# Performance work log

Measured on AMD Instinct MI355X. Metric: run time of the kernel, lower is better.

The kernel has to match this reference:

```python
import jax, jax.numpy as jnp
import numpy as np

B, N, D, H, E, W, OUT = 4, 2048, 128, 4, 32768, 8, 128


def setup_inputs() -> dict:
    key = jax.random.key(0)
    ks = jax.random.split(key, 11)
    s = 0.05  # weight init scale
    return {
        "nodefeatures": jax.random.normal(ks[0], (B, N, D), jnp.float32),
        "node_indices": jax.random.randint(ks[1], (B, 2, E), 0, N),
        "nodeattributes": jax.random.uniform(ks[2], (B, E, W), jnp.float32),
        "wq_w": jax.random.normal(ks[3], (H, D, D), jnp.float32) * s,
        "wq_b": jax.random.normal(ks[4], (H, D), jnp.float32) * s,
        "wk_w": jax.random.normal(ks[5], (H, D, D), jnp.float32) * s,
        "wk_b": jax.random.normal(ks[6], (H, D), jnp.float32) * s,
        "wv_w": jax.random.normal(ks[7], (H, D, D), jnp.float32) * s,
        "wv_b": jax.random.normal(ks[8], (H, D), jnp.float32) * s,
        "out_w": jax.random.normal(ks[9], (OUT, H * D), jnp.float32) * s,
        "out_b": jax.random.normal(ks[10], (OUT,), jnp.float32) * s,
    }


def reference(nodefeatures, node_indices, nodeattributes,
              wq_w, wq_b, wk_w, wk_b, wv_w, wv_b, out_w, out_b):
    b, n, d = nodefeatures.shape
    h = wq_w.shape[0]
    # per-head Linear projections: y = x @ W.T + bias, batched over heads -> [b,h,n,d]
    q = jnp.einsum('bnd,hed->bhne', nodefeatures, wq_w) + wq_b[None, :, None, :]
    k = jnp.einsum('bnd,hed->bhne', nodefeatures, wk_w) + wk_b[None, :, None, :]
    v = jnp.einsum('bnd,hed->bhne', nodefeatures, wv_w) + wv_b[None, :, None, :]

    i = node_indices[:, 0, :]  # [b,E] row indices
    j = node_indices[:, 1, :]  # [b,E] col indices

    # gather q_i, k_j per edge -> [b,h,E,d]; edge score = <q_i,k_j>/sqrt(n)
    qi = jnp.take_along_axis(q, i[:, None, :, None], axis=2)
    kj = jnp.take_along_axis(k, j[:, None, :, None], axis=2)
    wsum = nodeattributes.sum(axis=-1)  # [b,E] (x_edge[:,None]*weights).sum(1)
    # original divides by k.shape[1]**0.5 == sqrt(n)
    edge = (qi * kj).sum(-1) / (n ** 0.5) * wsum[:, None, :]  # [b,h,E]

    # scatter edge scores into zero-initialized dense logits [b,h,n,n]
    bi = jnp.arange(b)[:, None, None]
    hi = jnp.arange(h)[None, :, None]
    scores = jnp.zeros((b, h, n, n), q.dtype).at[bi, hi, i[:, None, :], j[:, None, :]].set(edge)

    attn = jax.nn.softmax(scores, axis=-1)
    o = jnp.einsum('bhnm,bhmd->bhnd', attn, v)
    o = o.transpose(0, 2, 1, 3).reshape(b, n, h * d)  # concat heads on feature dim
    return o @ out_w.T + out_b
```

## Files before the change

kernel.cpp:

```cpp
#include <hip/hip_runtime.h>
#include <hip/hip_bf16.h>
#include <math.h>

constexpr int B_ = 4;
constexpr int N_ = 2048;
constexpr int D_ = 128;
constexpr int H_ = 4;
constexpr int E_ = 32768;
constexpr int W_ = 8;
constexpr int OUT_ = 128;
constexpr int HD_ = H_ * D_;
constexpr int C3_ = 3 * HD_;
constexpr int CAP = 64;
constexpr int M_ = B_ * N_;

typedef __attribute__((ext_vector_type(8))) __bf16 bf16x8;
typedef __attribute__((ext_vector_type(4))) float f32x4;
typedef unsigned int uint32;
typedef unsigned short u16;

__device__ __forceinline__ u16 f2b(float f) {
    __hip_bfloat16 h = __float2bfloat16(f);
    return *(u16*)&h;
}
__device__ __forceinline__ float blo(uint32 u) { return __uint_as_float(u << 16); }
__device__ __forceinline__ float bhi(uint32 u) { return __uint_as_float(u & 0xffff0000u); }

__device__ __forceinline__ void g2l16(const void* g, void* l) {
    __builtin_amdgcn_global_load_lds(
        (const __attribute__((address_space(1))) unsigned int*)(uintptr_t)g,
        (__attribute__((address_space(3))) unsigned int*)(uintptr_t)l,
        16, 0, 0);
}

__global__ __launch_bounds__(256) void prep_kernel(
    const float* __restrict__ X,
    const float* __restrict__ wq, const float* __restrict__ wk, const float* __restrict__ wv,
    const float* __restrict__ bq, const float* __restrict__ bk, const float* __restrict__ bv,
    const float* __restrict__ OW,
    u16* __restrict__ Xbf, u16* __restrict__ Wbf, float* __restrict__ biasf,
    u16* __restrict__ OWbf,
    int* __restrict__ row_count, float* __restrict__ vsum)
{
    const int blk = blockIdx.x;
    if (blk < 512) {
        const int tid = blk * 256 + threadIdx.x;
        const float4 f0 = *(const float4*)(X + (size_t)tid * 8);
        const float4 f1 = *(const float4*)(X + (size_t)tid * 8 + 4);
        union { u16 u[8]; uint4 v; } pk;
        pk.u[0]=f2b(f0.x); pk.u[1]=f2b(f0.y); pk.u[2]=f2b(f0.z); pk.u[3]=f2b(f0.w);
        pk.u[4]=f2b(f1.x); pk.u[5]=f2b(f1.y); pk.u[6]=f2b(f1.z); pk.u[7]=f2b(f1.w);
        *(uint4*)((char*)Xbf + (size_t)tid * 16) = pk.v;
    } else if (blk < 608) {
        const int c = (blk - 512) * 256 + threadIdx.x;
        const int g = c >> 11, idx = c & 2047;
        const int t3 = g >> 2, h = g & 3;
        const float* Wsrc = (t3 == 0 ? wq : t3 == 1 ? wk : wv) + (size_t)h * 128 * 128;
        const float4 f0 = *(const float4*)(Wsrc + (size_t)idx * 8);
        const float4 f1 = *(const float4*)(Wsrc + (size_t)idx * 8 + 4);
        union { u16 u[8]; uint4 v; } pk;
        pk.u[0]=f2b(f0.x); pk.u[1]=f2b(f0.y); pk.u[2]=f2b(f0.z); pk.u[3]=f2b(f0.w);
        pk.u[4]=f2b(f1.x); pk.u[5]=f2b(f1.y); pk.u[6]=f2b(f1.z); pk.u[7]=f2b(f1.w);
        *(uint4*)((char*)Wbf + (size_t)c * 16) = pk.v;
        if (idx < 128) {
            const float* Bsrc = (t3 == 0 ? bq : t3 == 1 ? bk : bv) + h * 128;
            biasf[g * 128 + idx] = Bsrc[idx];
        }
    } else if (blk < 640) {
        const int tid = (blk - 608) * 256 + threadIdx.x;
        const int c = tid >> 6, sub = tid & 63;
        const float4 f0 = *(const float4*)(OW + (size_t)c * 512 + sub * 8);
        const float4 f1 = *(const float4*)(OW + (size_t)c * 512 + sub * 8 + 4);
        union { u16 u[8]; uint4 v; } pk;
        pk.u[0]=f2b(f0.x); pk.u[1]=f2b(f0.y); pk.u[2]=f2b(f0.z); pk.u[3]=f2b(f0.w);
        pk.u[4]=f2b(f1.x); pk.u[5]=f2b(f1.y); pk.u[6]=f2b(f1.z); pk.u[7]=f2b(f1.w);
        const int ob = c * 1024 + ((sub * 16) ^ ((c & 7) << 4));
        *(uint4*)((char*)OWbf + ob) = pk.v;
    } else {
        const uint4 z = make_uint4(0, 0, 0, 0);
        uint4* rc = (uint4*)row_count;
        #pragma unroll
        for (int q = 0; q < 8; ++q) rc[threadIdx.x + q * 256] = z;
        uint4* vs = (uint4*)vsum;
        #pragma unroll
        for (int q = 0; q < 2; ++q) vs[threadIdx.x + q * 256] = z;
    }
}

__global__ __launch_bounds__(256) void qkv_append(
    const u16* __restrict__ Xbf, const u16* __restrict__ Wbf,
    const float* __restrict__ biasf,
    const int* __restrict__ nidx, const float* __restrict__ attr,
    u16* __restrict__ QKV, float* __restrict__ vsum,
    int* __restrict__ row_count, int2* __restrict__ row_edges)
{
    __shared__ u16 Cs[128 * 128];
    const int t = threadIdx.x;
    const int lane = t & 63, wave = t >> 6;

    if (blockIdx.x >= 768) {
        const int gw = (blockIdx.x - 768) * 4 + wave;
        const int e0g = gw * 8;
        const int b = e0g / E_;
        const int e0 = e0g % E_;
        float a = attr[((size_t)b * E_ + e0) * W_ + lane];
        a += __shfl_xor(a, 1);
        a += __shfl_xor(a, 2);
        a += __shfl_xor(a, 4);
        if ((lane & 7) == 0) {
            const int sub = lane >> 3;
            const int e = e0 + sub;
            const int i = nidx[b * 2 * E_ + e];
            const int j = nidx[b * 2 * E_ + E_ + e];
            const int pos = atomicAdd(&row_count[b * N_ + i], 1);
            if (pos < CAP)
                row_edges[(size_t)(b * N_ + i) * CAP + pos] =
                    make_int2(e | (j << 16), __float_as_int(a));
        }
        return;
    }

    const int rb = blockIdx.x & 63;
    const int g  = blockIdx.x >> 6;
    const int wm = wave >> 1, wn = wave & 1;
    const int l15 = lane & 15, l4 = lane >> 4;

    const u16* Abase = Xbf + (size_t)(rb * 128) * 128;
    const u16* Bbase = Wbf + (size_t)(g  * 128) * 128;

    f32x4 acc[4][4];
    #pragma unroll
    for (int i = 0; i < 4; ++i)
        #pragma unroll
        for (int j = 0; j < 4; ++j) acc[i][j] = (f32x4){0.f, 0.f, 0.f, 0.f};

    #pragma unroll
    for (int ks = 0; ks < 4; ++ks) {
        const int ko = ks * 32 + l4 * 8;
        bf16x8 a[4], bb[4];
        #pragma unroll
        for (int fm = 0; fm < 4; ++fm)
            a[fm] = *(const bf16x8*)(Abase + (wm * 64 + fm * 16 + l15) * 128 + ko);
        #pragma unroll
        for (int fn = 0; fn < 4; ++fn)
            bb[fn] = *(const bf16x8*)(Bbase + (wn * 64 + fn * 16 + l15) * 128 + ko);
        #pragma unroll
        for (int fm = 0; fm < 4; ++fm)
            #pragma unroll
            for (int fn = 0; fn < 4; ++fn)
                acc[fm][fn] = __builtin_amdgcn_mfma_f32_16x16x32_bf16(
                    a[fm], bb[fn], acc[fm][fn], 0, 0, 0);
    }

    #pragma unroll
    for (int fm = 0; fm < 4; ++fm)
        #pragma unroll
        for (int fn = 0; fn < 4; ++fn) {
            const int col = wn * 64 + fn * 16 + l15;
            const float bv = biasf[g * 128 + col];
            #pragma unroll
            for (int r = 0; r < 4; ++r) {
                const int row = wm * 64 + fm * 16 + l4 * 4 + r;
                *(u16*)((char*)Cs + row * 256 + ((col * 2) ^ ((row & 7) << 4))) =
                    f2b(acc[fm][fn][r] + bv);
            }
        }

    if (g >= 8) {
        const int h = g - 8;
        const int b = rb >> 4;
        #pragma unroll
        for (int fn = 0; fn < 4; ++fn) {
            float s = 0.f;
            #pragma unroll
            for (int fm = 0; fm < 4; ++fm)
                #pragma unroll
                for (int r = 0; r < 4; ++r) s += acc[fm][fn][r];
            s += __shfl_xor(s, 16);
            s += __shfl_xor(s, 32);
            if (l4 == 0) {
                const int col = wn * 64 + fn * 16 + l15;
                const float bv = biasf[g * 128 + col];
                atomicAdd(&vsum[(b * H_ + h) * 128 + col], s + 64.f * bv);
            }
        }
    }
    __syncthreads();

    #pragma unroll
    for (int q = 0; q < 8; ++q) {
        const int idx = t + q * 256;
        const int row = idx >> 4, c = idx & 15;
        const uint4 v = *(const uint4*)((char*)Cs + row * 256 + ((c * 16) ^ ((row & 7) << 4)));
        *(uint4*)(QKV + (size_t)(rb * 128 + row) * C3_ + g * 128 + c * 8) = v;
    }
}

__global__ __launch_bounds__(256) void row_fused(
    const u16* __restrict__ QKV, const float* __restrict__ vsum,
    const int* __restrict__ row_count, const int2* __restrict__ row_edges,
    u16* __restrict__ Obf)
{
    const int t = threadIdx.x;
    const int wave = t >> 6, lane = t & 63;
    const int rid = wave >> 1, half = wave & 1;
    const int row = blockIdx.x * 2 + rid;
    const int b = blockIdx.y;
    const int R = b * N_ + row;
    int cnt = row_count[R];
    if (cnt > CAP) cnt = CAP;

    int ej = 0; float ws = 0.f;
    if (lane < cnt) {
        const int2 v = row_edges[(size_t)R * CAP + lane];
        ej = v.x; ws = __int_as_float(v.y);
    }
    const int myj = ej >> 16, mye = ej & 0xFFFF;
    bool win = (lane < cnt);
    for (int p = 0; p < cnt; ++p) {
        const int oj = __shfl(ej, p);
        if (win && (oj >> 16) == myj && (oj & 0xFFFF) > mye) win = false;
    }
    const unsigned long long wmask = __ballot(win);
    const int pos = (int)__popcll(wmask & ((1ull << lane) - 1ull));
    unsigned long long m = __ballot(win && ((pos & 1) == half));

    const char* base = (const char*)QKV;
    const uint4 qv = *(const uint4*)(base + (size_t)R * 3072 + lane * 16);
    const float q0=blo(qv.x), q1=bhi(qv.x), q2=blo(qv.y), q3=bhi(qv.y),
                q4=blo(qv.z), q5=bhi(qv.z), q6=blo(qv.w), q7=bhi(qv.w);
    const float rs = 0.02209708691207961f;

    float A0=0.f,A1=0.f,A2=0.f,A3=0.f,A4=0.f,A5=0.f,A6=0.f,A7=0.f;
    float B0=0.f,B1=0.f,B2=0.f,B3=0.f,B4=0.f,B5=0.f,B6=0.f,B7=0.f;
    float dsA = 0.f, dsB = 0.f;

#define FETCH(MM, KV1,VV1,W1,KV2,VV2,W2,NN)                                  \
    { int p_ = (int)__ffsll((long long)MM) - 1; MM &= MM - 1;                \
      const int j_ = __shfl(ej, p_) >> 16; W1 = __shfl(ws, p_);              \
      const char* nb_ = base + (size_t)(b * N_ + j_) * 3072;                 \
      KV1 = *(const uint4*)(nb_ + 1024 + lane * 16);                         \
      VV1 = *(const uint4*)(nb_ + 2048 + lane * 16);                         \
      if (MM) {                                                              \
        int q_ = (int)__ffsll((long long)MM) - 1; MM &= MM - 1;              \
        const int j2_ = __shfl(ej, q_) >> 16; W2 = __shfl(ws, q_);           \
        const char* nb2_ = base + (size_t)(b * N_ + j2_) * 3072;             \
        KV2 = *(const uint4*)(nb2_ + 1024 + lane * 16);                      \
        VV2 = *(const uint4*)(nb2_ + 2048 + lane * 16);                      \
        NN = 2;                                                              \
      } else NN = 1; }

#define PROC(kv, vv, wsp, S)                                                 \
    { float s_ = q0*blo(kv.x) + q1*bhi(kv.x) + q2*blo(kv.y) + q3*bhi(kv.y)   \
               + q4*blo(kv.z) + q5*bhi(kv.z) + q6*blo(kv.w) + q7*bhi(kv.w);  \
      s_ += __shfl_xor(s_, 1);                                               \
      s_ += __shfl_xor(s_, 2);                                               \
      s_ += __shfl_xor(s_, 4);                                               \
      s_ += __shfl_xor(s_, 8);                                               \
      const float x_ = expf(s_ * rs * (wsp)) - 1.f;                          \
      ds##S += x_;                                                           \
      S##0 = fmaf(x_, blo(vv.x), S##0); S##1 = fmaf(x_, bhi(vv.x), S##1);    \
      S##2 = fmaf(x_, blo(vv.y), S##2); S##3 = fmaf(x_, bhi(vv.y), S##3);    \
      S##4 = fmaf(x_, blo(vv.z), S##4); S##5 = fmaf(x_, bhi(vv.z), S##5);    \
      S##6 = fmaf(x_, blo(vv.w), S##6); S##7 = fmaf(x_, bhi(vv.w), S##7); }

    if (m) {
        uint4 kv1, vv1, kv2, vv2; float w1, w2; int n1;
        FETCH(m, kv1, vv1, w1, kv2, vv2, w2, n1);
        while (m) {
            uint4 nk1, nv1, nk2, nv2; float nw1, nw2; int n2;
            FETCH(m, nk1, nv1, nw1, nk2, nv2, nw2, n2);
            PROC(kv1, vv1, w1, A);
            if (n1 == 2) PROC(kv2, vv2, w2, B);
            kv1 = nk1; vv1 = nv1; w1 = nw1;
            kv2 = nk2; vv2 = nv2; w2 = nw2; n1 = n2;
        }
        PROC(kv1, vv1, w1, A);
        if (n1 == 2) PROC(kv2, vv2, w2, B);
    }
#undef FETCH
#undef PROC

    __shared__ float part[2][64][9];
    if (half == 1) {
        float* p = part[rid][lane];
        p[0]=A0+B0; p[1]=A1+B1; p[2]=A2+B2; p[3]=A3+B3;
        p[4]=A4+B4; p[5]=A5+B5; p[6]=A6+B6; p[7]=A7+B7;
        p[8]=dsA+dsB;
    }
    __syncthreads();
    if (half == 0) {
        const float* p = part[rid][lane];
        const float o0=A0+B0+p[0], o1=A1+B1+p[1], o2=A2+B2+p[2], o3=A3+B3+p[3];
        const float o4=A4+B4+p[4], o5=A5+B5+p[5], o6=A6+B6+p[6], o7=A7+B7+p[7];
        const float inv = 1.0f / (2048.0f + dsA + dsB + p[8]);
        const float* vsp = vsum + (b * H_ + (lane >> 4)) * 128 + (lane & 15) * 8;
        const float4 vs0 = *(const float4*)vsp;
        const float4 vs1 = *(const float4*)(vsp + 4);
        union { u16 u[8]; uint4 v; } o;
        o.u[0]=f2b((vs0.x+o0)*inv); o.u[1]=f2b((vs0.y+o1)*inv);
        o.u[2]=f2b((vs0.z+o2)*inv); o.u[3]=f2b((vs0.w+o3)*inv);
        o.u[4]=f2b((vs1.x+o4)*inv); o.u[5]=f2b((vs1.y+o5)*inv);
        o.u[6]=f2b((vs1.z+o6)*inv); o.u[7]=f2b((vs1.w+o7)*inv);
        const int ob = ((lane >> 4) << 8) + (((lane & 15) * 16) ^ ((R & 7) << 4));
        *(uint4*)((char*)Obf + (size_t)R * 1024 + ob) = o.v;
    }
}

__global__ __launch_bounds__(256) void out_mfma(
    const u16* __restrict__ Obf, const u16* __restrict__ OWbf,
    const float* __restrict__ bo, float* __restrict__ Out)
{
    __shared__ u16 As[32 * 128];
    __shared__ u16 Bs[128 * 128];
    const int rb = blockIdx.x;
    const int t = threadIdx.x;
    const int lane = t & 63, wave = t >> 6;
    const int wm = wave >> 1, wn = wave & 1;
    const int l15 = lane & 15, l4 = lane >> 4;

    f32x4 acc[4];
    #pragma unroll
    for (int j = 0; j < 4; ++j) acc[j] = (f32x4){0.f, 0.f, 0.f, 0.f};

    for (int kc = 0; kc < 4; ++kc) {
        #pragma unroll
        for (int q = 0; q < 2; ++q) {
            const int o = t * 16 + q * 4096;
            const int arow = o >> 8, ob = o & 255;
            g2l16((const char*)Obf + (size_t)(rb * 32 + arow) * 1024 + kc * 256 + ob,
                  (char*)As + o);
        }
        #pragma unroll
        for (int q = 0; q < 8; ++q) {
            const int o = t * 16 + q * 4096;
            const int c = o >> 8, ob = o & 255;
            g2l16((const char*)OWbf + (size_t)c * 1024 + kc * 256 + ob,
                  (char*)Bs + o);
        }
        __syncthreads();
        #pragma unroll
        for (int ks = 0; ks < 4; ++ks) {
            const int kb = ks * 64 + l4 * 16;
            bf16x8 a0, bb[4];
            {
                const int row = wm * 16 + l15;
                a0 = *(const bf16x8*)((const char*)As + row * 256 + (kb ^ ((row & 7) << 4)));
            }
            #pragma unroll
            for (int fn = 0; fn < 4; ++fn) {
                const int col = wn * 64 + fn * 16 + l15;
                bb[fn] = *(const bf16x8*)((const char*)Bs + col * 256 + (kb ^ ((col & 7) << 4)));
            }
            #pragma unroll
            for (int fn = 0; fn < 4; ++fn)
                acc[fn] = __builtin_amdgcn_mfma_f32_16x16x32_bf16(
                    a0, bb[fn], acc[fn], 0, 0, 0);
        }
        __syncthreads();
    }

    #pragma unroll
    for (int fn = 0; fn < 4; ++fn) {
        const int col = wn * 64 + fn * 16 + l15;
        const float bv = bo[col];
        #pragma unroll
        for (int r = 0; r < 4; ++r) {
            const int row = rb * 32 + wm * 16 + l4 * 4 + r;
            Out[(size_t)row * OUT_ + col] = acc[fn][r] + bv;
        }
    }
}

extern "C" void kernel_launch(void* const* d_in, const int* in_sizes, int n_in,
                              void* d_out, int out_size, void* d_ws, size_t ws_size,
                              hipStream_t stream)
{
    const float* x     = (const float*)d_in[0];
    const int*   nidx  = (const int*)  d_in[1];
    const float* attr  = (const float*)d_in[2];
    const float* wq_w  = (const float*)d_in[3];
    const float* wq_b  = (const float*)d_in[4];
    const float* wk_w  = (const float*)d_in[5];
    const float* wk_b  = (const float*)d_in[6];
    const float* wv_w  = (const float*)d_in[7];
    const float* wv_b  = (const float*)d_in[8];
    const float* out_w = (const float*)d_in[9];
    const float* out_b = (const float*)d_in[10];
    float* out = (float*)d_out;

    char* ws = (char*)d_ws;
    size_t off = 0;
    auto alloc = [&](size_t bytes) -> char* {
        char* p = ws + off;
        off += (bytes + 255) & ~(size_t)255;
        return p;
    };
    u16*  Xbf  = (u16*)alloc((size_t)M_ * D_ * 2);
    u16*  Wbf  = (u16*)alloc((size_t)12 * D_ * D_ * 2);
    float* biasf = (float*)alloc((size_t)12 * D_ * 4);
    u16*  QKV  = (u16*)alloc((size_t)M_ * C3_ * 2);
    u16*  OWbf = (u16*)alloc((size_t)OUT_ * HD_ * 2);
    u16*  Obf  = (u16*)alloc((size_t)M_ * HD_ * 2);
    float* vsum = (float*)alloc((size_t)B_ * H_ * D_ * 4);
    int*  row_count = (int*)alloc((size_t)B_ * N_ * 4);
    int2* row_edges = (int2*)alloc((size_t)B_ * N_ * CAP * 8);

    prep_kernel<<<641, 256, 0, stream>>>(
        x, wq_w, wk_w, wv_w, wq_b, wk_b, wv_b, out_w,
        Xbf, Wbf, biasf, OWbf, row_count, vsum);
    qkv_append<<<768 + 4096, 256, 0, stream>>>(
        Xbf, Wbf, biasf, nidx, attr, QKV, vsum, row_count, row_edges);
    row_fused<<<dim3(N_ / 2, B_), 256, 0, stream>>>(
        QKV, vsum, row_count, row_edges, Obf);
    out_mfma<<<M_ / 32, 256, 0, stream>>>(Obf, OWbf, out_b, out);
}
```

Before: 81.15 us.

## Use one wave per row and map batches to XCD pairs in row_fused

Each row is now handled by a single wave instead of two waves splitting the edges, which removes the LDS partial-sum exchange and the block barrier. Block IDs are remapped so that all rows of one batch land on the same pair of XCDs, keeping that batch's gathered K/V rows local to fewer L2 caches. In exchange, per-row latency grows because one wave processes every edge serially, and there is less memory-level parallelism per row.

```diff
diff --git a/kernel.cpp b/kernel.cpp
--- a/kernel.cpp
+++ b/kernel.cpp
@@ -203,9 +203,11 @@
 {
     const int t = threadIdx.x;
     const int wave = t >> 6, lane = t & 63;
-    const int rid = wave >> 1, half = wave & 1;
-    const int row = blockIdx.x * 2 + rid;
-    const int b = blockIdx.y;
+    const int gid = blockIdx.x;
+    const int xcd = gid & 7;
+    const int b = xcd >> 1;
+    const int rowgrp = ((xcd & 1) << 8) | (gid >> 3);
+    const int row = rowgrp * 4 + wave;
     const int R = b * N_ + row;
     int cnt = row_count[R];
     if (cnt > CAP) cnt = CAP;
@@ -221,9 +223,7 @@
         const int oj = __shfl(ej, p);
         if (win && (oj >> 16) == myj && (oj & 0xFFFF) > mye) win = false;
     }
-    const unsigned long long wmask = __ballot(win);
-    const int pos = (int)__popcll(wmask & ((1ull << lane) - 1ull));
-    unsigned long long m = __ballot(win && ((pos & 1) == half));
+    unsigned long long m = __ballot(win);
 
     const char* base = (const char*)QKV;
     const uint4 qv = *(const uint4*)(base + (size_t)R * 3072 + lane * 16);
@@ -281,30 +281,17 @@
 #undef FETCH
 #undef PROC
 
-    __shared__ float part[2][64][9];
-    if (half == 1) {
-        float* p = part[rid][lane];
-        p[0]=A0+B0; p[1]=A1+B1; p[2]=A2+B2; p[3]=A3+B3;
-        p[4]=A4+B4; p[5]=A5+B5; p[6]=A6+B6; p[7]=A7+B7;
-        p[8]=dsA+dsB;
-    }
-    __syncthreads();
-    if (half == 0) {
-        const float* p = part[rid][lane];
-        const float o0=A0+B0+p[0], o1=A1+B1+p[1], o2=A2+B2+p[2], o3=A3+B3+p[3];
-        const float o4=A4+B4+p[4], o5=A5+B5+p[5], o6=A6+B6+p[6], o7=A7+B7+p[7];
-        const float inv = 1.0f / (2048.0f + dsA + dsB + p[8]);
-        const float* vsp = vsum + (b * H_ + (lane >> 4)) * 128 + (lane & 15) * 8;
-        const float4 vs0 = *(const float4*)vsp;
-        const float4 vs1 = *(const float4*)(vsp + 4);
-        union { u16 u[8]; uint4 v; } o;
-        o.u[0]=f2b((vs0.x+o0)*inv); o.u[1]=f2b((vs0.y+o1)*inv);
-        o.u[2]=f2b((vs0.z+o2)*inv); o.u[3]=f2b((vs0.w+o3)*inv);
-        o.u[4]=f2b((vs1.x+o4)*inv); o.u[5]=f2b((vs1.y+o5)*inv);
-        o.u[6]=f2b((vs1.z+o6)*inv); o.u[7]=f2b((vs1.w+o7)*inv);
-        const int ob = ((lane >> 4) << 8) + (((lane & 15) * 16) ^ ((R & 7) << 4));
-        *(uint4*)((char*)Obf + (size_t)R * 1024 + ob) = o.v;
-    }
+    const float inv = 1.0f / (2048.0f + dsA + dsB);
+    const float* vsp = vsum + (b * H_ + (lane >> 4)) * 128 + (lane & 15) * 8;
+    const float4 vs0 = *(const float4*)vsp;
+    const float4 vs1 = *(const float4*)(vsp + 4);
+    union { u16 u[8]; uint4 v; } o;
+    o.u[0]=f2b((vs0.x+A0+B0)*inv); o.u[1]=f2b((vs0.y+A1+B1)*inv);
+    o.u[2]=f2b((vs0.z+A2+B2)*inv); o.u[3]=f2b((vs0.w+A3+B3)*inv);
+    o.u[4]=f2b((vs1.x+A4+B4)*inv); o.u[5]=f2b((vs1.y+A5+B5)*inv);
+    o.u[6]=f2b((vs1.z+A6+B6)*inv); o.u[7]=f2b((vs1.w+A7+B7)*inv);
+    const int ob = ((lane >> 4) << 8) + (((lane & 15) * 16) ^ ((R & 7) << 4));
+    *(uint4*)((char*)Obf + (size_t)R * 1024 + ob) = o.v;
 }
 
 __global__ __launch_bounds__(256) void out_mfma(
@@ -411,7 +398,7 @@
         Xbf, Wbf, biasf, OWbf, row_count, vsum);
     qkv_append<<<768 + 4096, 256, 0, stream>>>(
         Xbf, Wbf, biasf, nidx, attr, QKV, vsum, row_count, row_edges);
-    row_fused<<<dim3(N_ / 2, B_), 256, 0, stream>>>(
+    row_fused<<<2048, 256, 0, stream>>>(
         QKV, vsum, row_count, row_edges, Obf);
     out_mfma<<<M_ / 32, 256, 0, stream>>>(Obf, OWbf, out_b, out);
 }
```

After: 77.87 us. 4.0% less time.
